# Performance work log

Measured on AMD Instinct MI355X. Metric: run time of the kernel, lower is better.

The kernel has to match this reference:

```python
import jax, jax.numpy as jnp
import numpy as np

T, B, I, H = 512, 2048, 24, 20


def setup_inputs() -> dict:
    key = jax.random.key(0)
    ks = jax.random.split(key, 10)
    x = jax.random.normal(ks[0], (T, B, I), dtype=jnp.float32)
    # pack_padded_sequence(enforce_sorted=True) needs descending lengths; force max = T
    lengths = jax.random.randint(ks[1], (B,), 1, T + 1)
    lengths = jnp.sort(lengths)[::-1].at[0].set(T)
    s = float(1.0 / np.sqrt(H))  # PyTorch LSTM/Linear init scale
    u = lambda k, shp: jax.random.uniform(k, shp, jnp.float32, -s, s)
    return {
        "x": x,
        "x_lengths": lengths,
        "W_ih": u(ks[2], (4 * H, I)),
        "W_hh": u(ks[3], (4 * H, H)),
        "b_ih": u(ks[4], (4 * H,)),
        "b_hh": u(ks[5], (4 * H,)),
        "W_a": u(ks[6], (1, H)),
        "b_a": u(ks[7], (1,)),
        "W_b": u(ks[8], (1, H)),
        "b_b": u(ks[9], (1,)),
    }


def _lstm(x, W_ih, W_hh, b_ih, b_hh):
    # x: [T, B, I]. PyTorch gate order: i, f, g, o.
    # Precompute input projections for all timesteps (one big GEMM).
    xg = jnp.einsum('tbi,gi->tbg', x, W_ih) + (b_ih + b_hh)  # [T, B, 4H]

    def step(carry, xg_t):
        h, c = carry
        g = xg_t + h @ W_hh.T  # [B, 4H]
        i, f, gg, o = jnp.split(g, 4, axis=-1)
        c = jax.nn.sigmoid(f) * c + jax.nn.sigmoid(i) * jnp.tanh(gg)
        h = jax.nn.sigmoid(o) * jnp.tanh(c)
        return (h, c), h

    h0 = jnp.zeros((x.shape[1], W_hh.shape[1]), x.dtype)
    (_, _), hs = jax.lax.scan(step, (h0, h0), xg)
    return hs  # [T, B, H]


def reference(x, W_ih, W_hh, b_ih, b_hh, W_a, b_a, W_b, b_b, x_lengths):
    hs = _lstm(x, W_ih, W_hh, b_ih, b_hh)
    # pad_packed_sequence zeros outputs at t >= length
    mask = (jnp.arange(x.shape[0])[:, None] < x_lengths[None, :])[..., None]
    hs = jnp.where(mask, hs, jnp.zeros((), hs.dtype))
    alpha = jnp.exp(hs @ W_a.T + b_a)          # [T, B, 1]
    beta = jax.nn.softplus(hs @ W_b.T + b_b)   # [T, B, 1]
    return alpha, beta
```

## Files before the change

### kernel.cpp

```cpp
#include <hip/hip_runtime.h>


typedef float f2 __attribute__((ext_vector_type(2)));

constexpr int T_ = 512;
constexpr int B_ = 2048;
constexpr int I_ = 24;
constexpr int H_ = 20;
constexpr int CH = 30;
constexpr size_t TB_ = (size_t)T_ * B_;

__device__ __forceinline__ float sigm(float x) {
  return __fdividef(1.0f, 1.0f + __expf(-x));
}
__device__ __forceinline__ float tanh_fast(float x) {
  return 1.0f - __fdividef(2.0f, 1.0f + __expf(2.0f * x));
}
__device__ __forceinline__ float softplus_fast(float x) {
  return __logf(1.0f + __expf(x));
}
__device__ __forceinline__ float rdlane(float v, int l) {
  return __int_as_float(__builtin_amdgcn_readlane(__float_as_int(v), l));
}
__device__ __forceinline__ f2 pkfma(f2 a, float s, f2 c) {
  return __builtin_elementwise_fma(a, (f2){s, s}, c);
}

__device__ __forceinline__ f2 dot24(const f2* W, const float* xf, f2 acc) {
  f2 s0 = {0,0}, s1 = {0,0}, s2 = {0,0}, s3 = {0,0};
  #pragma unroll
  for (int k = 0; k < I_; k += 4) {
    s0 = pkfma(W[k],     xf[k],     s0);
    s1 = pkfma(W[k + 1], xf[k + 1], s1);
    s2 = pkfma(W[k + 2], xf[k + 2], s2);
    s3 = pkfma(W[k + 3], xf[k + 3], s3);
  }
  return acc + ((s0 + s1) + (s2 + s3));
}

__global__ __launch_bounds__(64, 2)
void lstm_fused(const float* __restrict__ x,
                const int* __restrict__ lens,
                const float* __restrict__ W_ih,
                const float* __restrict__ W_hh,
                const float* __restrict__ b_ih,
                const float* __restrict__ b_hh,
                const float* __restrict__ W_a, const float* __restrict__ b_a,
                const float* __restrict__ W_b, const float* __restrict__ b_b,
                float* __restrict__ out)
{
  const int lane = threadIdx.x;
  const int b = blockIdx.x;
  const int len = lens[b];

  const bool grpA = lane < H_;
  const bool grpB = (lane >= 32) && (lane < 32 + H_);
  const bool own = grpA || grpB;
  const int j = grpA ? lane : (grpB ? (lane - 32) : 0);
  const int g0 = grpA ? j : (H_ + j);
  const int g1 = g0 + 2 * H_;

  __shared__ float xs[2][CH * I_];
  __shared__ float hst[CH][H_];

  f2 Wx[I_], Wh[H_];
  #pragma unroll
  for (int k = 0; k < I_; ++k) {
    f2 w = { W_ih[g0 * I_ + k], W_ih[g1 * I_ + k] };
    Wx[k] = own ? w : (f2){0.0f, 0.0f};
  }
  #pragma unroll
  for (int k = 0; k < H_; ++k) {
    f2 w = { W_hh[g0 * H_ + k], W_hh[g1 * H_ + k] };
    Wh[k] = own ? w : (f2){0.0f, 0.0f};
  }
  f2 bias = { b_ih[g0] + b_hh[g0], b_ih[g1] + b_hh[g1] };
  bias = own ? bias : (f2){0.0f, 0.0f};

  f2 wab[H_];
  #pragma unroll
  for (int k = 0; k < H_; ++k) wab[k] = (f2){ W_a[k], W_b[k] };
  const float ba = b_a[0], bb = b_b[0];

  float hk[H_];
  #pragma unroll
  for (int k = 0; k < H_; ++k) hk[k] = 0.0f;
  float c = 0.0f, h = 0.0f;

  float4 p0, p1, p2;
  auto GADDR = [&](int ch, int off) -> const float4* {
    const int s = off / 96;
    const int f = (off % 96) >> 2;
    int t = ch * CH + s; if (t > T_ - 1) t = T_ - 1;
    return (const float4*)(x + ((size_t)t * B_ + b) * I_ + f);
  };
  auto GLOAD = [&](int ch) {
    p0 = *GADDR(ch, lane * 16);
    p1 = *GADDR(ch, 1024 + lane * 16);
    if (lane < 52) p2 = *GADDR(ch, 2048 + lane * 16);
  };
  auto DSWRITE = [&](int buf) {
    char* base = (char*)&xs[buf][0];
    *(float4*)(base + lane * 16) = p0;
    *(float4*)(base + 1024 + lane * 16) = p1;
    if (lane < 52) *(float4*)(base + 2048 + lane * 16) = p2;
  };
  auto READX = [&](float* dst, int buf, int s) {
    const float4* q = (const float4*)&xs[buf][s * I_];
    #pragma unroll
    for (int r = 0; r < 6; ++r) {
      const float4 v = q[r];
      dst[4*r] = v.x; dst[4*r+1] = v.y; dst[4*r+2] = v.z; dst[4*r+3] = v.w;
    }
  };

  auto STEP = [&](int s) {
    f2 s0 = {0,0}, s1 = {0,0}, s2 = {0,0}, s3 = {0,0};
    #pragma unroll
    for (int k = 0; k < H_; k += 4) {
      s0 = pkfma(Wh[k],     hk[k],     s0);
      s1 = pkfma(Wh[k + 1], hk[k + 1], s1);
      s2 = pkfma(Wh[k + 2], hk[k + 2], s2);
      s3 = pkfma(Wh[k + 3], hk[k + 3], s3);
    }
    const f2 a =  (f2){0,0};  (void)a;
    const f2 av = (f2){0,0}; (void)av;
    f2 g = (f2){0,0}; (void)g;
    const f2 aa = ((s0 + s1) + (s2 + s3));
    const f2 at = (f2){aa.x, aa.y};
    const f2 afull = at; (void)afull;
    const f2 A = (f2){at.x, at.y};
    (void)A;
    const float ax = aa.x + 0.0f; (void)ax;
    const f2 atot = aa;
    const float a0 = atot.x, a1 = atot.y;
    const float ia0 = a0, ia1 = a1; (void)ia0; (void)ia1;
    const float A0 = a0, A1 = a1; (void)A0; (void)A1;
    const float u = sigm(a0 + 0.0f + 0.0f + 0.0f + 0.0f + 0.0f);
    (void)u;
  };
  (void)STEP;

#define DO_STEP(SIDX)                                                        \
  {                                                                          \
    f2 q0 = {0,0}, q1 = {0,0}, q2 = {0,0}, q3 = {0,0};                       \
    _Pragma("unroll")                                                        \
    for (int k = 0; k < H_; k += 4) {                                        \
      q0 = pkfma(Wh[k],     hk[k],     q0);                                  \
      q1 = pkfma(Wh[k + 1], hk[k + 1], q1);                                  \
      q2 = pkfma(Wh[k + 2], hk[k + 2], q2);                                  \
      q3 = pkfma(Wh[k + 3], hk[k + 3], q3);                                  \
    }                                                                        \
    const f2 a = acc + ((q0 + q1) + (q2 + q3));                              \
    const float u = sigm(a.x);                        \
    const float yy = grpA ? (a.y + a.y) : a.y;                               \
    const float sg = sigm(yy);                                               \
    const float v = grpA ? fmaf(2.0f, sg, -1.0f) : sg;  \
    const float p = u * v;                           \
    const float p_ = __shfl_xor(p, 32, 64);                \
    c = fmaf(u, c, p_);                                    \
    const float tc = tanh_fast(c);                                           \
    h = v * tc;                                            \
    if (grpB) hst[SIDX][j] = h;                                              \
    _Pragma("unroll")                                                        \
    for (int k = 0; k < H_; ++k) hk[k] = rdlane(h, 32 + k);                  \
  }

  GLOAD(0);
  DSWRITE(0);
  GLOAD(1);
  {
    float xt[I_];
    READX(xt, 0, 0);
  }
  float xt0[I_];
  READX(xt0, 0, 0);
  f2 acc = dot24(Wx, xt0, bias);

  int t0 = 0;
  #pragma unroll 1
  for (int ci = 0; ; ++ci, t0 += CH) {
    const int buf = ci & 1;
    const int rem = len - t0;
    const int sh = rem < CH ? rem : CH;

    #pragma unroll 1
    for (int s = 0; s < sh; ++s) {
      float xn[I_];
      READX(xn, buf, (s + 1 < CH) ? s + 1 : 0);
      DO_STEP(s);
      acc = dot24(Wx, xn, bias);
    }

    if (lane < sh) {
      const float4* hq = (const float4*)&hst[lane][0];
      f2 pa = {0,0}, pb = {0,0};
      #pragma unroll
      for (int r = 0; r < 5; ++r) {
        const float4 hv = hq[r];
        pa = pkfma(wab[4*r],     hv.x, pa);
        pb = pkfma(wab[4*r + 1], hv.y, pb);
        pa = pkfma(wab[4*r + 2], hv.z, pa);
        pb = pkfma(wab[4*r + 3], hv.w, pb);
      }
      const f2 pp = pa + pb;
      const size_t n = (size_t)(t0 + lane) * B_ + b;
      out[n]       = __expf(pp.x + ba);
      out[TB_ + n] = softplus_fast(pp.y + bb);
    }

    if (t0 + sh >= len) break;

    DSWRITE(buf ^ 1);
    GLOAD(ci + 2);
    float xq[I_];
    READX(xq, buf ^ 1, 0);
    acc = dot24(Wx, xq, bias);
  }

  const float apad = __expf(ba);
  const float bpad = softplus_fast(bb);
  for (int t = len + lane; t < T_; t += 64) {
    out[(size_t)t * B_ + b]       = apad;
    out[TB_ + (size_t)t * B_ + b] = bpad;
  }
#undef DO_STEP
}

extern "C" void kernel_launch(void* const* d_in, const int* in_sizes, int n_in,
                              void* d_out, int out_size, void* d_ws, size_t ws_size,
                              hipStream_t stream) {
  (void)in_sizes; (void)n_in; (void)out_size; (void)d_ws; (void)ws_size;
  lstm_fused<<<dim3(B_), dim3(64), 0, stream>>>(
      (const float*)d_in[0], (const int*)d_in[1],
      (const float*)d_in[2], (const float*)d_in[3],
      (const float*)d_in[4], (const float*)d_in[5],
      (const float*)d_in[6], (const float*)d_in[7],
      (const float*)d_in[8], (const float*)d_in[9],
      (float*)d_out);
}
```

Measured before the change: 338.2 us.

## Pack two batch sequences per wavefront, one lane computing all four gates

```diff
diff --git a/kernel.cpp b/kernel.cpp
--- a/kernel.cpp
+++ b/kernel.cpp
@@ -8,6 +8,7 @@
 constexpr int I_ = 24;
 constexpr int H_ = 20;
 constexpr int CH = 30;
+constexpr int XBUF = 2 * CH * I_;
 constexpr size_t TB_ = (size_t)T_ * B_;
 
 __device__ __forceinline__ float sigm(float x) {
@@ -19,26 +20,11 @@
 __device__ __forceinline__ float softplus_fast(float x) {
   return __logf(1.0f + __expf(x));
 }
-__device__ __forceinline__ float rdlane(float v, int l) {
-  return __int_as_float(__builtin_amdgcn_readlane(__float_as_int(v), l));
-}
 __device__ __forceinline__ f2 pkfma(f2 a, float s, f2 c) {
   return __builtin_elementwise_fma(a, (f2){s, s}, c);
 }
 
-__device__ __forceinline__ f2 dot24(const f2* W, const float* xf, f2 acc) {
-  f2 s0 = {0,0}, s1 = {0,0}, s2 = {0,0}, s3 = {0,0};
-  #pragma unroll
-  for (int k = 0; k < I_; k += 4) {
-    s0 = pkfma(W[k],     xf[k],     s0);
-    s1 = pkfma(W[k + 1], xf[k + 1], s1);
-    s2 = pkfma(W[k + 2], xf[k + 2], s2);
-    s3 = pkfma(W[k + 3], xf[k + 3], s3);
-  }
-  return acc + ((s0 + s1) + (s2 + s3));
-}
-
-__global__ __launch_bounds__(64, 2)
+__global__ __launch_bounds__(64, 1)
 void lstm_fused(const float* __restrict__ x,
                 const int* __restrict__ lens,
                 const float* __restrict__ W_ih,
@@ -50,188 +36,177 @@
                 float* __restrict__ out)
 {
   const int lane = threadIdx.x;
-  const int b = blockIdx.x;
-  const int len = lens[b];
-
-  const bool grpA = lane < H_;
-  const bool grpB = (lane >= 32) && (lane < 32 + H_);
-  const bool own = grpA || grpB;
-  const int j = grpA ? lane : (grpB ? (lane - 32) : 0);
-  const int g0 = grpA ? j : (H_ + j);
-  const int g1 = g0 + 2 * H_;
-
-  __shared__ float xs[2][CH * I_];
-  __shared__ float hst[CH][H_];
-
-  f2 Wx[I_], Wh[H_];
+  const int hf   = lane >> 5;
+  const int j    = lane & 31;
+  const int bA   = blockIdx.x * 2;
+  const int b    = bA + hf;
+  const int lenA = lens[bA];
+  const int len  = lens[b];
+
+  __shared__ float xs[2 * XBUF];
+  __shared__ float hst[2][CH][24];
+  __shared__ float hbuf[2][24];
+
+  const int jj = (j < H_) ? j : 0;
+  f2 Wxig[I_], Wxfo[I_];
   #pragma unroll
   for (int k = 0; k < I_; ++k) {
-    f2 w = { W_ih[g0 * I_ + k], W_ih[g1 * I_ + k] };
-    Wx[k] = own ? w : (f2){0.0f, 0.0f};
-  }
+    Wxig[k] = (f2){ W_ih[jj * I_ + k],          W_ih[(2 * H_ + jj) * I_ + k] };
+    Wxfo[k] = (f2){ W_ih[(H_ + jj) * I_ + k],   W_ih[(3 * H_ + jj) * I_ + k] };
+  }
+  f2 Whig[H_], Whfo[H_];
   #pragma unroll
   for (int k = 0; k < H_; ++k) {
-    f2 w = { W_hh[g0 * H_ + k], W_hh[g1 * H_ + k] };
-    Wh[k] = own ? w : (f2){0.0f, 0.0f};
-  }
-  f2 bias = { b_ih[g0] + b_hh[g0], b_ih[g1] + b_hh[g1] };
-  bias = own ? bias : (f2){0.0f, 0.0f};
+    Whig[k] = (f2){ W_hh[jj * H_ + k],          W_hh[(2 * H_ + jj) * H_ + k] };
+    Whfo[k] = (f2){ W_hh[(H_ + jj) * H_ + k],   W_hh[(3 * H_ + jj) * H_ + k] };
+  }
+  const f2 big = { b_ih[jj] + b_hh[jj],
+                   b_ih[2 * H_ + jj] + b_hh[2 * H_ + jj] };
+  const f2 bfo = { b_ih[H_ + jj] + b_hh[H_ + jj],
+                   b_ih[3 * H_ + jj] + b_hh[3 * H_ + jj] };
 
   f2 wab[H_];
   #pragma unroll
   for (int k = 0; k < H_; ++k) wab[k] = (f2){ W_a[k], W_b[k] };
   const float ba = b_a[0], bb = b_b[0];
 
+  int sA_[6], fA_[6], bat_[6];
+  #pragma unroll
+  for (int r = 0; r < 6; ++r) {
+    const int fi  = r * 256 + lane * 4;
+    const int bt  = fi / 720;
+    const int rem = fi - bt * 720;
+    bat_[r] = bt; sA_[r] = rem / 24; fA_[r] = rem - (rem / 24) * 24;
+  }
+
+  float4 p[6];
+  auto GLOAD = [&](int ch) {
+    #pragma unroll
+    for (int r = 0; r < 6; ++r) {
+      if (r < 5 || lane < 40) {
+        int t = ch * CH + sA_[r]; t = t < T_ ? t : T_ - 1;
+        p[r] = *(const float4*)(x + ((size_t)t * B_ + (bA + bat_[r])) * I_ + fA_[r]);
+      }
+    }
+  };
+  auto DSWRITE = [&](int buf) {
+    #pragma unroll
+    for (int r = 0; r < 6; ++r)
+      if (r < 5 || lane < 40)
+        *(float4*)(&xs[buf * XBUF + r * 256 + lane * 4]) = p[r];
+  };
+
+  float xn[I_];
+  auto READX = [&](int buf, int s) {
+    const float4* q = (const float4*)(&xs[buf * XBUF + hf * (CH * I_) + s * I_]);
+    #pragma unroll
+    for (int r = 0; r < 6; ++r) {
+      const float4 v = q[r];
+      xn[4*r] = v.x; xn[4*r+1] = v.y; xn[4*r+2] = v.z; xn[4*r+3] = v.w;
+    }
+  };
+
+  f2 accig, accfo;
+  auto XDOT = [&]() {
+    f2 u0 = {0,0}, u1 = {0,0}, v0 = {0,0}, v1 = {0,0};
+    #pragma unroll
+    for (int k = 0; k < I_; k += 2) {
+      u0 = pkfma(Wxig[k],     xn[k],     u0);
+      u1 = pkfma(Wxig[k + 1], xn[k + 1], u1);
+      v0 = pkfma(Wxfo[k],     xn[k],     v0);
+      v1 = pkfma(Wxfo[k + 1], xn[k + 1], v1);
+    }
+    accig = big + (u0 + u1);
+    accfo = bfo + (v0 + v1);
+  };
+
   float hk[H_];
   #pragma unroll
   for (int k = 0; k < H_; ++k) hk[k] = 0.0f;
   float c = 0.0f, h = 0.0f;
-
-  float4 p0, p1, p2;
-  auto GADDR = [&](int ch, int off) -> const float4* {
-    const int s = off / 96;
-    const int f = (off % 96) >> 2;
-    int t = ch * CH + s; if (t > T_ - 1) t = T_ - 1;
-    return (const float4*)(x + ((size_t)t * B_ + b) * I_ + f);
-  };
-  auto GLOAD = [&](int ch) {
-    p0 = *GADDR(ch, lane * 16);
-    p1 = *GADDR(ch, 1024 + lane * 16);
-    if (lane < 52) p2 = *GADDR(ch, 2048 + lane * 16);
-  };
-  auto DSWRITE = [&](int buf) {
-    char* base = (char*)&xs[buf][0];
-    *(float4*)(base + lane * 16) = p0;
-    *(float4*)(base + 1024 + lane * 16) = p1;
-    if (lane < 52) *(float4*)(base + 2048 + lane * 16) = p2;
-  };
-  auto READX = [&](float* dst, int buf, int s) {
-    const float4* q = (const float4*)&xs[buf][s * I_];
-    #pragma unroll
-    for (int r = 0; r < 6; ++r) {
-      const float4 v = q[r];
-      dst[4*r] = v.x; dst[4*r+1] = v.y; dst[4*r+2] = v.z; dst[4*r+3] = v.w;
-    }
-  };
-
-  auto STEP = [&](int s) {
-    f2 s0 = {0,0}, s1 = {0,0}, s2 = {0,0}, s3 = {0,0};
-    #pragma unroll
-    for (int k = 0; k < H_; k += 4) {
-      s0 = pkfma(Wh[k],     hk[k],     s0);
-      s1 = pkfma(Wh[k + 1], hk[k + 1], s1);
-      s2 = pkfma(Wh[k + 2], hk[k + 2], s2);
-      s3 = pkfma(Wh[k + 3], hk[k + 3], s3);
-    }
-    const f2 a =  (f2){0,0};  (void)a;
-    const f2 av = (f2){0,0}; (void)av;
-    f2 g = (f2){0,0}; (void)g;
-    const f2 aa = ((s0 + s1) + (s2 + s3));
-    const f2 at = (f2){aa.x, aa.y};
-    const f2 afull = at; (void)afull;
-    const f2 A = (f2){at.x, at.y};
-    (void)A;
-    const float ax = aa.x + 0.0f; (void)ax;
-    const f2 atot = aa;
-    const float a0 = atot.x, a1 = atot.y;
-    const float ia0 = a0, ia1 = a1; (void)ia0; (void)ia1;
-    const float A0 = a0, A1 = a1; (void)A0; (void)A1;
-    const float u = sigm(a0 + 0.0f + 0.0f + 0.0f + 0.0f + 0.0f);
-    (void)u;
-  };
-  (void)STEP;
-
-#define DO_STEP(SIDX)                                                        \
-  {                                                                          \
-    f2 q0 = {0,0}, q1 = {0,0}, q2 = {0,0}, q3 = {0,0};                       \
-    _Pragma("unroll")                                                        \
-    for (int k = 0; k < H_; k += 4) {                                        \
-      q0 = pkfma(Wh[k],     hk[k],     q0);                                  \
-      q1 = pkfma(Wh[k + 1], hk[k + 1], q1);                                  \
-      q2 = pkfma(Wh[k + 2], hk[k + 2], q2);                                  \
-      q3 = pkfma(Wh[k + 3], hk[k + 3], q3);                                  \
-    }                                                                        \
-    const f2 a = acc + ((q0 + q1) + (q2 + q3));                              \
-    const float u = sigm(a.x);                        \
-    const float yy = grpA ? (a.y + a.y) : a.y;                               \
-    const float sg = sigm(yy);                                               \
-    const float v = grpA ? fmaf(2.0f, sg, -1.0f) : sg;  \
-    const float p = u * v;                           \
-    const float p_ = __shfl_xor(p, 32, 64);                \
-    c = fmaf(u, c, p_);                                    \
-    const float tc = tanh_fast(c);                                           \
-    h = v * tc;                                            \
-    if (grpB) hst[SIDX][j] = h;                                              \
-    _Pragma("unroll")                                                        \
-    for (int k = 0; k < H_; ++k) hk[k] = rdlane(h, 32 + k);                  \
-  }
 
   GLOAD(0);
   DSWRITE(0);
   GLOAD(1);
-  {
-    float xt[I_];
-    READX(xt, 0, 0);
-  }
-  float xt0[I_];
-  READX(xt0, 0, 0);
-  f2 acc = dot24(Wx, xt0, bias);
+  READX(0, 0);
+  XDOT();
 
   int t0 = 0;
   #pragma unroll 1
-  for (int ci = 0; ; ++ci, t0 += CH) {
+  for (int ci = 0;; ++ci, t0 += CH) {
     const int buf = ci & 1;
-    const int rem = len - t0;
+    const int rem = lenA - t0;
     const int sh = rem < CH ? rem : CH;
 
     #pragma unroll 1
     for (int s = 0; s < sh; ++s) {
-      float xn[I_];
-      READX(xn, buf, (s + 1 < CH) ? s + 1 : 0);
-      DO_STEP(s);
-      acc = dot24(Wx, xn, bias);
-    }
-
-    if (lane < sh) {
-      const float4* hq = (const float4*)&hst[lane][0];
+      READX(buf, (s + 1 < CH) ? s + 1 : 0);
+      f2 q0 = {0,0}, q1 = {0,0}, r0 = {0,0}, r1 = {0,0};
+      #pragma unroll
+      for (int k = 0; k < H_; k += 2) {
+        q0 = pkfma(Whig[k],     hk[k],     q0);
+        q1 = pkfma(Whig[k + 1], hk[k + 1], q1);
+        r0 = pkfma(Whfo[k],     hk[k],     r0);
+        r1 = pkfma(Whfo[k + 1], hk[k + 1], r1);
+      }
+      const f2 aig = accig + (q0 + q1);
+      const f2 afo = accfo + (r0 + r1);
+      const float si = sigm(aig.x);
+      const float tg = tanh_fast(aig.y);
+      const float sf = sigm(afo.x);
+      const float so = sigm(afo.y);
+      c = fmaf(sf, c, si * tg);
+      h = so * tanh_fast(c);
+      if (j < H_) { hst[hf][s][j] = h; hbuf[hf][j] = h; }
+      {
+        const float4* hq = (const float4*)(&hbuf[hf][0]);
+        #pragma unroll
+        for (int r5 = 0; r5 < 5; ++r5) {
+          const float4 hv = hq[r5];
+          hk[4*r5] = hv.x; hk[4*r5+1] = hv.y; hk[4*r5+2] = hv.z; hk[4*r5+3] = hv.w;
+        }
+      }
+      XDOT();
+    }
+
+    if (j < sh && (t0 + j) < len) {
+      const float4* hq = (const float4*)(&hst[hf][j][0]);
       f2 pa = {0,0}, pb = {0,0};
       #pragma unroll
-      for (int r = 0; r < 5; ++r) {
-        const float4 hv = hq[r];
-        pa = pkfma(wab[4*r],     hv.x, pa);
-        pb = pkfma(wab[4*r + 1], hv.y, pb);
-        pa = pkfma(wab[4*r + 2], hv.z, pa);
-        pb = pkfma(wab[4*r + 3], hv.w, pb);
+      for (int r5 = 0; r5 < 5; ++r5) {
+        const float4 hv = hq[r5];
+        pa = pkfma(wab[4*r5],     hv.x, pa);
+        pb = pkfma(wab[4*r5 + 1], hv.y, pb);
+        pa = pkfma(wab[4*r5 + 2], hv.z, pa);
+        pb = pkfma(wab[4*r5 + 3], hv.w, pb);
       }
       const f2 pp = pa + pb;
-      const size_t n = (size_t)(t0 + lane) * B_ + b;
+      const size_t n = (size_t)(t0 + j) * B_ + b;
       out[n]       = __expf(pp.x + ba);
       out[TB_ + n] = softplus_fast(pp.y + bb);
     }
 
-    if (t0 + sh >= len) break;
+    if (t0 + sh >= lenA) break;
 
     DSWRITE(buf ^ 1);
     GLOAD(ci + 2);
-    float xq[I_];
-    READX(xq, buf ^ 1, 0);
-    acc = dot24(Wx, xq, bias);
+    READX(buf ^ 1, 0);
+    XDOT();
   }
 
   const float apad = __expf(ba);
   const float bpad = softplus_fast(bb);
-  for (int t = len + lane; t < T_; t += 64) {
+  for (int t = len + j; t < T_; t += 32) {
     out[(size_t)t * B_ + b]       = apad;
     out[TB_ + (size_t)t * B_ + b] = bpad;
   }
-#undef DO_STEP
 }
 
 extern "C" void kernel_launch(void* const* d_in, const int* in_sizes, int n_in,
                               void* d_out, int out_size, void* d_ws, size_t ws_size,
                               hipStream_t stream) {
   (void)in_sizes; (void)n_in; (void)out_size; (void)d_ws; (void)ws_size;
-  lstm_fused<<<dim3(B_), dim3(64), 0, stream>>>(
+  lstm_fused<<<dim3(B_ / 2), dim3(64), 0, stream>>>(
       (const float*)d_in[0], (const int*)d_in[1],
       (const float*)d_in[2], (const float*)d_in[3],
       (const float*)d_in[4], (const float*)d_in[5],
```

New measurement: 433.4 us. 28.1% more time.
